# Performance work log

Measured on AMD Instinct MI355X. Metric: run time of the kernel, lower is better.

Reference implementation:

```python
import jax, jax.numpy as jnp
import numpy as np

N = 100000
E = 600000
IN_DIM = 128
HID = 128


def setup_inputs() -> dict:
    key = jax.random.key(0)
    ks = jax.random.split(key, 12)
    def lin(kw, fan_in, fan_out):
        # torch nn.Linear default init: U(-1/sqrt(fan_in), 1/sqrt(fan_in))
        bound = 1.0 / np.sqrt(fan_in)
        kw1, kw2 = jax.random.split(kw)
        w = jax.random.uniform(kw1, (fan_in, fan_out), jnp.float32, -bound, bound)
        b = jax.random.uniform(kw2, (fan_out,), jnp.float32, -bound, bound)
        return w, b
    x = jax.random.normal(ks[0], (N, IN_DIM), jnp.float32)
    edge_index = jax.random.randint(ks[1], (2, E), 0, N, jnp.int64)
    w1a, b1a = lin(ks[2], IN_DIM, HID)
    w1b, b1b = lin(ks[3], HID, HID)
    w2a, b2a = lin(ks[4], HID, HID)
    w2b, b2b = lin(ks[5], HID, HID)
    wo, bo = lin(ks[6], HID, 1)
    return {"x": x, "edge_index": edge_index,
            "w1a": w1a, "b1a": b1a, "w1b": w1b, "b1b": b1b,
            "w2a": w2a, "b2a": b2a, "w2b": w2b, "b2b": b2b,
            "wo": wo, "bo": bo}


def _gin_conv(x, src, dst, wa, ba, wb, bb):
    # sum-aggregate neighbor features: agg[dst] += x[src]; eps = 0 (GIN default)
    agg = jax.ops.segment_sum(x[src], dst, num_segments=N)
    h = x + agg
    h = jax.nn.relu(h @ wa + ba)
    return h @ wb + bb


def reference(x, edge_index, w1a, b1a, w1b, b1b, w2a, b2a, w2b, b2b, wo, bo):
    src, dst = edge_index[0], edge_index[1]
    h = _gin_conv(x, src, dst, w1a, b1a, w1b, b1b)
    h = _gin_conv(h, src, dst, w2a, b2a, w2b, b2b)
    return (h @ wo + bo).squeeze(-1)  # [N]
```

## Files before the change

kernel.cpp:

```cpp
#include <hip/hip_runtime.h>

typedef unsigned short u16;
typedef unsigned int u32;
typedef __bf16 bf16x8 __attribute__((ext_vector_type(8)));
typedef float f32x4 __attribute__((ext_vector_type(4)));

__device__ __forceinline__ u16 f2bf(float f) {
  union { float f; u32 u; } c; c.f = f;
  return (u16)((c.u + 0x7fffu + ((c.u >> 16) & 1u)) >> 16);
}
__device__ __forceinline__ float2 upk2(u32 v) {
  union { u32 u; float f; } a, b; a.u = v << 16; b.u = v & 0xffff0000u;
  return make_float2(a.f, b.f);
}
__device__ __forceinline__ u32 pk2(float x, float y) {
  return (u32)f2bf(x) | ((u32)f2bf(y) << 16);
}

__global__ __launch_bounds__(256) void k_cast(const float4* __restrict__ in,
                                              uint2* __restrict__ out, int n4) {
  int i = blockIdx.x * 256 + threadIdx.x;
  if (i < n4) {
    float4 v = in[i];
    out[i] = make_uint2(pk2(v.x, v.y), pk2(v.z, v.w));
  }
}

__global__ __launch_bounds__(256) void k_hist(const int* __restrict__ dst,
                                              int* __restrict__ counts, int E) {
  int e = blockIdx.x * 256 + threadIdx.x;
  if (e < E) atomicAdd(&counts[dst[e]], 1);
}

__global__ __launch_bounds__(256) void k_scan1(const int* __restrict__ counts,
                                               int* __restrict__ excl,
                                               int* __restrict__ partials, int n) {
  __shared__ int sh[256];
  int b = blockIdx.x, t = threadIdx.x;
  int base = b * 1024 + t * 4;
  int v[4];
#pragma unroll
  for (int j = 0; j < 4; ++j) { int i = base + j; v[j] = (i < n) ? counts[i] : 0; }
  int tot = v[0] + v[1] + v[2] + v[3];
  sh[t] = tot; __syncthreads();
  for (int off = 1; off < 256; off <<= 1) {
    int x = (t >= off) ? sh[t - off] : 0;
    __syncthreads();
    sh[t] += x;
    __syncthreads();
  }
  int run = sh[t] - tot;
#pragma unroll
  for (int j = 0; j < 4; ++j) {
    int i = base + j;
    if (i < n) excl[i] = run;
    run += v[j];
  }
  if (t == 255) partials[b] = sh[255];
}

__global__ __launch_bounds__(128) void k_scan2(int* __restrict__ partials, int nb) {
  __shared__ int sh[128];
  int t = threadIdx.x;
  int v = (t < nb) ? partials[t] : 0;
  sh[t] = v; __syncthreads();
  for (int off = 1; off < 128; off <<= 1) {
    int x = (t >= off) ? sh[t - off] : 0;
    __syncthreads();
    sh[t] += x;
    __syncthreads();
  }
  if (t < nb) partials[t] = sh[t] - v;
}

__global__ __launch_bounds__(256) void k_scan3(int* __restrict__ rowstart,
                                               int* __restrict__ cursor,
                                               const int* __restrict__ partials,
                                               int n, int E) {
  int i = blockIdx.x * 256 + threadIdx.x;
  if (i < n) {
    int v = rowstart[i] + partials[i >> 10];
    rowstart[i] = v;
    cursor[i] = v;
  }
  if (i == 0) rowstart[n] = E;
}

__global__ __launch_bounds__(256) void k_fill(const int* __restrict__ src,
                                              const int* __restrict__ dst,
                                              int* __restrict__ cursor,
                                              int* __restrict__ edge_src, int E) {
  int e = blockIdx.x * 256 + threadIdx.x;
  if (e < E) {
    int d = dst[e];
    int pos = atomicAdd(&cursor[d], 1);
    edge_src[pos] = src[e];
  }
}

__global__ __launch_bounds__(256) void k_tr(const float* __restrict__ w0,
                                            const float* __restrict__ w1,
                                            const float* __restrict__ w2,
                                            const float* __restrict__ w3,
                                            u16* __restrict__ wT) {
  int id = blockIdx.x * 256 + threadIdx.x;
  int w = id >> 14, rem = id & 16383;
  int nn = rem >> 7, kk = rem & 127;
  const float* s = (w == 0) ? w0 : (w == 1) ? w1 : (w == 2) ? w2 : w3;
  wT[id] = f2bf(s[kk * 128 + nn]);
}

__global__ __launch_bounds__(256) void k_agg(const u32* __restrict__ in,
                                             u32* __restrict__ out,
                                             const int* __restrict__ rowstart,
                                             const int* __restrict__ edge_src, int N) {
  int node = __builtin_amdgcn_readfirstlane(blockIdx.x * 4 + (threadIdx.x >> 6));
  int lane = threadIdx.x & 63;
  if (node >= N) return;
  const u32* __restrict__ col = in + lane;
  float2 acc = upk2(col[node * 64]);
  int e0 = rowstart[node], e1 = rowstart[node + 1];
  for (int e = e0; e < e1; e += 8) {
    int idx[8]; float w[8]; u32 v[8];
#pragma unroll
    for (int j = 0; j < 8; ++j) {
      int ej = e + j;
      int c = (ej < e1) ? ej : (e1 - 1);
      idx[j] = edge_src[c];
      w[j] = (ej < e1) ? 1.f : 0.f;
    }
#pragma unroll
    for (int j = 0; j < 8; ++j) v[j] = col[idx[j] * 64];
#pragma unroll
    for (int j = 0; j < 8; ++j) {
      float2 p = upk2(v[j]);
      acc.x = fmaf(w[j], p.x, acc.x);
      acc.y = fmaf(w[j], p.y, acc.y);
    }
  }
  out[node * 64 + lane] = pk2(acc.x, acc.y);
}

template <bool HEAD>
__global__ __launch_bounds__(256) void k_mlp(const u16* __restrict__ in,
                                             const u16* __restrict__ wAT,
                                             const float* __restrict__ bA,
                                             const u16* __restrict__ wBT,
                                             const float* __restrict__ bB,
                                             const float* __restrict__ wo,
                                             const float* __restrict__ bo,
                                             void* __restrict__ outp, int N) {
  __shared__ u16 lA[64 * 128];
  __shared__ u16 lW[128 * 128];
  const int tid = threadIdx.x;
  const int wave = tid >> 6, lane = tid & 63;
  const int base = blockIdx.x * 64;

#pragma unroll
  for (int it = 0; it < 4; ++it) {
    int id = it * 256 + tid;
    int row = id >> 4, c = id & 15;
    uint4 v = make_uint4(0u, 0u, 0u, 0u);
    if (base + row < N) v = *(const uint4*)&in[(base + row) * 128 + c * 8];
    *(uint4*)&lA[row * 128 + ((c ^ (row & 15)) << 3)] = v;
  }
#pragma unroll
  for (int it = 0; it < 8; ++it) {
    int id = it * 256 + tid;
    int row = id >> 4, c = id & 15;
    uint4 v = *(const uint4*)&wAT[row * 128 + c * 8];
    *(uint4*)&lW[row * 128 + ((c ^ (row & 15)) << 3)] = v;
  }
  __syncthreads();

  const int m16 = lane & 15, quad = lane >> 4;
  const int mrow = wave * 16 + m16;

  bf16x8 aF[4];
#pragma unroll
  for (int ks = 0; ks < 4; ++ks)
    aF[ks] = *(const bf16x8*)&lA[mrow * 128 + (((ks * 4 + quad) ^ m16) << 3)];
  f32x4 acc[8];
#pragma unroll
  for (int t = 0; t < 8; ++t) acc[t] = (f32x4){0.f, 0.f, 0.f, 0.f};
#pragma unroll
  for (int t = 0; t < 8; ++t) {
    int nrow = t * 16 + m16;
#pragma unroll
    for (int ks = 0; ks < 4; ++ks) {
      bf16x8 bF = *(const bf16x8*)&lW[nrow * 128 + (((ks * 4 + quad) ^ m16) << 3)];
      acc[t] = __builtin_amdgcn_mfma_f32_16x16x32_bf16(aF[ks], bF, acc[t], 0, 0, 0);
    }
  }
  __syncthreads();

#pragma unroll
  for (int t = 0; t < 8; ++t) {
    int n = t * 16 + m16;
    float bias = bA[n];
#pragma unroll
    for (int r = 0; r < 4; ++r) {
      int rloc = quad * 4 + r;
      int absrow = wave * 16 + rloc;
      float v = acc[t][r] + bias;
      v = v > 0.f ? v : 0.f;
      lA[absrow * 128 + ((((n >> 3) ^ rloc) << 3) | (n & 7))] = f2bf(v);
    }
  }
#pragma unroll
  for (int it = 0; it < 8; ++it) {
    int id = it * 256 + tid;
    int row = id >> 4, c = id & 15;
    uint4 v = *(const uint4*)&wBT[row * 128 + c * 8];
    *(uint4*)&lW[row * 128 + ((c ^ (row & 15)) << 3)] = v;
  }
  __syncthreads();

#pragma unroll
  for (int ks = 0; ks < 4; ++ks)
    aF[ks] = *(const bf16x8*)&lA[mrow * 128 + (((ks * 4 + quad) ^ m16) << 3)];
#pragma unroll
  for (int t = 0; t < 8; ++t) acc[t] = (f32x4){0.f, 0.f, 0.f, 0.f};
#pragma unroll
  for (int t = 0; t < 8; ++t) {
    int nrow = t * 16 + m16;
#pragma unroll
    for (int ks = 0; ks < 4; ++ks) {
      bf16x8 bF = *(const bf16x8*)&lW[nrow * 128 + (((ks * 4 + quad) ^ m16) << 3)];
      acc[t] = __builtin_amdgcn_mfma_f32_16x16x32_bf16(aF[ks], bF, acc[t], 0, 0, 0);
    }
  }
#pragma unroll
  for (int t = 0; t < 8; ++t) {
    int n = t * 16 + m16;
    float bias = bB[n];
#pragma unroll
    for (int r = 0; r < 4; ++r) {
      int rloc = quad * 4 + r;
      int absrow = wave * 16 + rloc;
      float v = acc[t][r] + bias;
      lA[absrow * 128 + ((((n >> 3) ^ rloc) << 3) | (n & 7))] = f2bf(v);
    }
  }
  __syncthreads();

  if (!HEAD) {
    u16* out = (u16*)outp;
#pragma unroll
    for (int it = 0; it < 4; ++it) {
      int id = it * 256 + tid;
      int row = id >> 4, c = id & 15;
      if (base + row < N) {
        uint4 v = *(const uint4*)&lA[row * 128 + ((c ^ (row & 15)) << 3)];
        *(uint4*)&out[(base + row) * 128 + c * 8] = v;
      }
    }
  } else {
    float* out = (float*)outp;
    int row = tid >> 2, qh = tid & 3;
    float s = 0.f;
#pragma unroll
    for (int j = 0; j < 4; ++j) {
      int c = qh * 4 + j;
      uint4 v = *(const uint4*)&lA[row * 128 + ((c ^ (row & 15)) << 3)];
      const float* w = &wo[c * 8];
      float2 p;
      p = upk2(v.x); s += p.x * w[0] + p.y * w[1];
      p = upk2(v.y); s += p.x * w[2] + p.y * w[3];
      p = upk2(v.z); s += p.x * w[4] + p.y * w[5];
      p = upk2(v.w); s += p.x * w[6] + p.y * w[7];
    }
    s += __shfl_xor(s, 1, 64);
    s += __shfl_xor(s, 2, 64);
    if (qh == 0 && base + row < N) {
      out[base + row] = s + bo[0];
    }
  }
}

extern "C" void kernel_launch(void* const* d_in, const int* in_sizes, int n_in,
                              void* d_out, int out_size, void* d_ws, size_t ws_size,
                              hipStream_t stream) {
  const float* x = (const float*)d_in[0];
  const int* ei = (const int*)d_in[1];
  const int E = in_sizes[1] / 2;
  const int N = in_sizes[0] / 128;
  const int* srcI = ei;
  const int* dstI = ei + E;
  const float* w1a = (const float*)d_in[2];
  const float* b1a = (const float*)d_in[3];
  const float* w1b = (const float*)d_in[4];
  const float* b1b = (const float*)d_in[5];
  const float* w2a = (const float*)d_in[6];
  const float* b2a = (const float*)d_in[7];
  const float* w2b = (const float*)d_in[8];
  const float* b2b = (const float*)d_in[9];
  const float* wo = (const float*)d_in[10];
  const float* bo = (const float*)d_in[11];

  char* ws = (char*)d_ws;
  size_t off = 0;
  auto nx = [&](size_t bytes) {
    size_t o = off;
    off += (bytes + 511) & ~(size_t)511;
    return o;
  };
  int* cursor   = (int*)(ws + nx((size_t)N * 4));
  int* rowstart = (int*)(ws + nx((size_t)(N + 1) * 4));
  int* partials = (int*)(ws + nx(4096));
  int* edge_src = (int*)(ws + nx((size_t)E * 4));
  u16* wT       = (u16*)(ws + nx((size_t)4 * 16384 * 2));
  u16* xb       = (u16*)(ws + nx((size_t)N * 128 * 2));
  u16* bufA     = (u16*)(ws + nx((size_t)N * 128 * 2));
  u16* bufB     = (u16*)(ws + nx((size_t)N * 128 * 2));

  const int nb = (N + 1023) >> 10;

  hipMemsetAsync(cursor, 0, (size_t)N * 4, stream);
  k_hist<<<(E + 255) / 256, 256, 0, stream>>>(dstI, cursor, E);
  k_scan1<<<nb, 256, 0, stream>>>(cursor, rowstart, partials, N);
  k_scan2<<<1, 128, 0, stream>>>(partials, nb);
  k_scan3<<<(N + 255) / 256, 256, 0, stream>>>(rowstart, cursor, partials, N, E);
  k_fill<<<(E + 255) / 256, 256, 0, stream>>>(srcI, dstI, cursor, edge_src, E);
  k_tr<<<256, 256, 0, stream>>>(w1a, w1b, w2a, w2b, wT);

  const int n4 = N * 32;
  k_cast<<<(n4 + 255) / 256, 256, 0, stream>>>((const float4*)x, (uint2*)xb, n4);

  k_agg<<<(N + 3) / 4, 256, 0, stream>>>((const u32*)xb, (u32*)bufA, rowstart, edge_src, N);
  k_mlp<false><<<(N + 63) / 64, 256, 0, stream>>>(bufA, wT, b1a, wT + 16384, b1b,
                                                  nullptr, nullptr, bufB, N);
  k_agg<<<(N + 3) / 4, 256, 0, stream>>>((const u32*)bufB, (u32*)xb, rowstart, edge_src, N);
  k_mlp<true><<<(N + 63) / 64, 256, 0, stream>>>(xb, wT + 32768, b2a, wT + 49152, b2b,
                                                 wo, bo, d_out, N);
}
```

Measured before the change: 276.3 us.

## Fuse neighbor aggregation into MLP kernel, gathering directly into shared memory

```diff
diff --git a/kernel.cpp b/kernel.cpp
--- a/kernel.cpp
+++ b/kernel.cpp
@@ -110,46 +110,17 @@
   wT[id] = f2bf(s[kk * 128 + nn]);
 }
 
-__global__ __launch_bounds__(256) void k_agg(const u32* __restrict__ in,
-                                             u32* __restrict__ out,
-                                             const int* __restrict__ rowstart,
-                                             const int* __restrict__ edge_src, int N) {
-  int node = __builtin_amdgcn_readfirstlane(blockIdx.x * 4 + (threadIdx.x >> 6));
-  int lane = threadIdx.x & 63;
-  if (node >= N) return;
-  const u32* __restrict__ col = in + lane;
-  float2 acc = upk2(col[node * 64]);
-  int e0 = rowstart[node], e1 = rowstart[node + 1];
-  for (int e = e0; e < e1; e += 8) {
-    int idx[8]; float w[8]; u32 v[8];
-#pragma unroll
-    for (int j = 0; j < 8; ++j) {
-      int ej = e + j;
-      int c = (ej < e1) ? ej : (e1 - 1);
-      idx[j] = edge_src[c];
-      w[j] = (ej < e1) ? 1.f : 0.f;
-    }
-#pragma unroll
-    for (int j = 0; j < 8; ++j) v[j] = col[idx[j] * 64];
-#pragma unroll
-    for (int j = 0; j < 8; ++j) {
-      float2 p = upk2(v[j]);
-      acc.x = fmaf(w[j], p.x, acc.x);
-      acc.y = fmaf(w[j], p.y, acc.y);
-    }
-  }
-  out[node * 64 + lane] = pk2(acc.x, acc.y);
-}
-
 template <bool HEAD>
-__global__ __launch_bounds__(256) void k_mlp(const u16* __restrict__ in,
-                                             const u16* __restrict__ wAT,
-                                             const float* __restrict__ bA,
-                                             const u16* __restrict__ wBT,
-                                             const float* __restrict__ bB,
-                                             const float* __restrict__ wo,
-                                             const float* __restrict__ bo,
-                                             void* __restrict__ outp, int N) {
+__global__ __launch_bounds__(256) void k_fused(const u32* __restrict__ in,
+                                               const int* __restrict__ rowstart,
+                                               const int* __restrict__ edge_src,
+                                               const u16* __restrict__ wAT,
+                                               const float* __restrict__ bA,
+                                               const u16* __restrict__ wBT,
+                                               const float* __restrict__ bB,
+                                               const float* __restrict__ wo,
+                                               const float* __restrict__ bo,
+                                               void* __restrict__ outp, int N) {
   __shared__ u16 lA[64 * 128];
   __shared__ u16 lW[128 * 128];
   const int tid = threadIdx.x;
@@ -157,19 +128,81 @@
   const int base = blockIdx.x * 64;
 
 #pragma unroll
-  for (int it = 0; it < 4; ++it) {
-    int id = it * 256 + tid;
-    int row = id >> 4, c = id & 15;
-    uint4 v = make_uint4(0u, 0u, 0u, 0u);
-    if (base + row < N) v = *(const uint4*)&in[(base + row) * 128 + c * 8];
-    *(uint4*)&lA[row * 128 + ((c ^ (row & 15)) << 3)] = v;
-  }
-#pragma unroll
   for (int it = 0; it < 8; ++it) {
     int id = it * 256 + tid;
     int row = id >> 4, c = id & 15;
     uint4 v = *(const uint4*)&wAT[row * 128 + c * 8];
     *(uint4*)&lW[row * 128 + ((c ^ (row & 15)) << 3)] = v;
+  }
+
+  const u32* __restrict__ col = in + lane;
+  const int ldsw = ((lane >> 2) );
+  for (int i = 0; i < 8; ++i) {
+    int rA = wave * 16 + i, rB = rA + 8;
+    int nodeA = __builtin_amdgcn_readfirstlane(base + rA);
+    int nodeB = __builtin_amdgcn_readfirstlane(base + rB);
+    bool vA = nodeA < N, vB = nodeB < N;
+    float2 accA = make_float2(0.f, 0.f), accB = make_float2(0.f, 0.f);
+    int a0 = 0, a1 = 0, b0 = 0, b1 = 0;
+    if (vA) { a0 = rowstart[nodeA]; a1 = rowstart[nodeA + 1]; accA = upk2(col[(size_t)nodeA * 64]); }
+    if (vB) { b0 = rowstart[nodeB]; b1 = rowstart[nodeB + 1]; accB = upk2(col[(size_t)nodeB * 64]); }
+    int ea = a0, eb = b0;
+    while (ea < a1 && eb < b1) {
+      int ia[8], ib[8]; float wa[8], wb[8]; u32 va[8], vb[8];
+#pragma unroll
+      for (int j = 0; j < 8; ++j) {
+        int ej = ea + j; int c = (ej < a1) ? ej : (a1 - 1);
+        ia[j] = edge_src[c]; wa[j] = (ej < a1) ? 1.f : 0.f;
+        int fj = eb + j; int d = (fj < b1) ? fj : (b1 - 1);
+        ib[j] = edge_src[d]; wb[j] = (fj < b1) ? 1.f : 0.f;
+      }
+#pragma unroll
+      for (int j = 0; j < 8; ++j) { va[j] = col[(size_t)ia[j] * 64]; vb[j] = col[(size_t)ib[j] * 64]; }
+#pragma unroll
+      for (int j = 0; j < 8; ++j) {
+        float2 p = upk2(va[j]);
+        accA.x = fmaf(wa[j], p.x, accA.x); accA.y = fmaf(wa[j], p.y, accA.y);
+        float2 q = upk2(vb[j]);
+        accB.x = fmaf(wb[j], q.x, accB.x); accB.y = fmaf(wb[j], q.y, accB.y);
+      }
+      ea += 8; eb += 8;
+    }
+    while (ea < a1) {
+      int ia[8]; float wa[8]; u32 va[8];
+#pragma unroll
+      for (int j = 0; j < 8; ++j) {
+        int ej = ea + j; int c = (ej < a1) ? ej : (a1 - 1);
+        ia[j] = edge_src[c]; wa[j] = (ej < a1) ? 1.f : 0.f;
+      }
+#pragma unroll
+      for (int j = 0; j < 8; ++j) va[j] = col[(size_t)ia[j] * 64];
+#pragma unroll
+      for (int j = 0; j < 8; ++j) {
+        float2 p = upk2(va[j]);
+        accA.x = fmaf(wa[j], p.x, accA.x); accA.y = fmaf(wa[j], p.y, accA.y);
+      }
+      ea += 8;
+    }
+    while (eb < b1) {
+      int ib[8]; float wb[8]; u32 vb[8];
+#pragma unroll
+      for (int j = 0; j < 8; ++j) {
+        int fj = eb + j; int d = (fj < b1) ? fj : (b1 - 1);
+        ib[j] = edge_src[d]; wb[j] = (fj < b1) ? 1.f : 0.f;
+      }
+#pragma unroll
+      for (int j = 0; j < 8; ++j) vb[j] = col[(size_t)ib[j] * 64];
+#pragma unroll
+      for (int j = 0; j < 8; ++j) {
+        float2 q = upk2(vb[j]);
+        accB.x = fmaf(wb[j], q.x, accB.x); accB.y = fmaf(wb[j], q.y, accB.y);
+      }
+      eb += 8;
+    }
+    if (vA)
+      *(u32*)&lA[rA * 128 + (((ldsw ^ (rA & 15)) << 3) | ((lane & 3) << 1))] = pk2(accA.x, accA.y);
+    if (vB)
+      *(u32*)&lA[rB * 128 + (((ldsw ^ (rB & 15)) << 3) | ((lane & 3) << 1))] = pk2(accB.x, accB.y);
   }
   __syncthreads();
 
@@ -311,7 +344,6 @@
   int* edge_src = (int*)(ws + nx((size_t)E * 4));
   u16* wT       = (u16*)(ws + nx((size_t)4 * 16384 * 2));
   u16* xb       = (u16*)(ws + nx((size_t)N * 128 * 2));
-  u16* bufA     = (u16*)(ws + nx((size_t)N * 128 * 2));
   u16* bufB     = (u16*)(ws + nx((size_t)N * 128 * 2));
 
   const int nb = (N + 1023) >> 10;
@@ -327,10 +359,11 @@
   const int n4 = N * 32;
   k_cast<<<(n4 + 255) / 256, 256, 0, stream>>>((const float4*)x, (uint2*)xb, n4);
 
-  k_agg<<<(N + 3) / 4, 256, 0, stream>>>((const u32*)xb, (u32*)bufA, rowstart, edge_src, N);
-  k_mlp<false><<<(N + 63) / 64, 256, 0, stream>>>(bufA, wT, b1a, wT + 16384, b1b,
-                                                  nullptr, nullptr, bufB, N);
-  k_agg<<<(N + 3) / 4, 256, 0, stream>>>((const u32*)bufB, (u32*)xb, rowstart, edge_src, N);
-  k_mlp<true><<<(N + 63) / 64, 256, 0, stream>>>(xb, wT + 32768, b2a, wT + 49152, b2b,
-                                                 wo, bo, d_out, N);
-}
+  const int nblk = (N + 63) / 64;
+  k_fused<false><<<nblk, 256, 0, stream>>>((const u32*)xb, rowstart, edge_src,
+                                           wT, b1a, wT + 16384, b1b,
+                                           nullptr, nullptr, bufB, N);
+  k_fused<true><<<nblk, 256, 0, stream>>>((const u32*)bufB, rowstart, edge_src,
+                                          wT + 32768, b2a, wT + 49152, b2b,
+                                          wo, bo, d_out, N);
+}
```

Result: slower. 306.1 us (+10.8%).
